# Kernel optimization log

Hardware: AMD Instinct MI355X
Metric: run time of the kernel (lower is better)

The kernel has to match this reference:

```python
import jax, jax.numpy as jnp
import numpy as np

D_MODEL = 1024
D_FF = 4096
NUM_EXPERTS = 8
TOP_K = 2


def setup_inputs() -> dict:
    key = jax.random.key(0)
    ks = jax.random.split(key, 9)
    s_in = 1.0 / np.sqrt(D_MODEL)
    s_ff = 1.0 / np.sqrt(D_FF)
    return {
        "x": jax.random.normal(ks[0], (2, 1024, D_MODEL), dtype=jnp.float32),
        "Wg": jax.random.uniform(ks[1], (D_MODEL, NUM_EXPERTS), minval=-s_in, maxval=s_in, dtype=jnp.float32),
        "bg": jax.random.uniform(ks[2], (NUM_EXPERTS,), minval=-s_in, maxval=s_in, dtype=jnp.float32),
        "W1": jax.random.uniform(ks[3], (NUM_EXPERTS, D_MODEL, D_FF), minval=-s_in, maxval=s_in, dtype=jnp.float32),
        "b1": jax.random.uniform(ks[4], (NUM_EXPERTS, D_FF), minval=-s_in, maxval=s_in, dtype=jnp.float32),
        "W2": jax.random.uniform(ks[5], (NUM_EXPERTS, D_MODEL, D_FF), minval=-s_in, maxval=s_in, dtype=jnp.float32),
        "b2": jax.random.uniform(ks[6], (NUM_EXPERTS, D_FF), minval=-s_in, maxval=s_in, dtype=jnp.float32),
        "W3": jax.random.uniform(ks[7], (NUM_EXPERTS, D_FF, D_MODEL), minval=-s_ff, maxval=s_ff, dtype=jnp.float32),
        "b3": jax.random.uniform(ks[8], (NUM_EXPERTS, D_MODEL), minval=-s_ff, maxval=s_ff, dtype=jnp.float32),
    }


def reference(x, Wg, bg, W1, b1, W2, b2, W3, b3):
    B, S, D = x.shape
    xf = x.reshape(-1, D)                                   # [N, D]
    N = xf.shape[0]

    # ---- Router (eval mode: no noise) ----
    logits = xf @ Wg + bg                                   # [N, E]
    top_logits, top_idx = jax.lax.top_k(logits, TOP_K)      # [N, K]
    top_w = jax.nn.softmax(top_logits, axis=-1)             # softmax over the top-k logits
    # scatter top-k weights into dense [N, E]; indices are unique per row
    comb_w = jnp.zeros_like(logits).at[jnp.arange(N)[:, None], top_idx].set(top_w)

    # ---- Experts: GLU-MLP, dense per-expert (weights are 0 for unrouted tokens) ----
    h1 = jnp.einsum('nd,edf->enf', xf, W1) + b1[:, None, :]  # [E, N, F]
    h2 = jnp.einsum('nd,edf->enf', xf, W2) + b2[:, None, :]
    hidden = jax.nn.gelu(h1, approximate=False) * h2         # torch nn.GELU is exact (erf)
    expert_out = jnp.einsum('enf,efd->end', hidden, W3) + b3[:, None, :]  # [E, N, D]

    # ---- Weighted combine ----
    final = jnp.einsum('end,ne->nd', expert_out, comb_w)     # [N, D]
    aux_loss = 0.0  # eval mode: aux loss inactive
    return final.reshape(B, S, D), aux_loss
```

## Files before the change

### kernel.cpp

```cpp
#include <hip/hip_runtime.h>
#include <hip/hip_bf16.h>
#include <math.h>

#define D_MODEL 1024
#define D_FF    4096
#define NE      8
#define MT      256

typedef __bf16 bf16x8 __attribute__((ext_vector_type(8)));
typedef float  f32x4  __attribute__((ext_vector_type(4)));

__device__ __forceinline__ void async16(const void* g, void* l) {
    __builtin_amdgcn_global_load_lds(
        (__attribute__((address_space(1))) uint32_t*)g,
        (__attribute__((address_space(3))) uint32_t*)l, 16, 0, 0);
}

__device__ __forceinline__ void transpose_tile_k128(
    const float* __restrict__ s, __bf16* __restrict__ d,
    int K, int N, int kt, int nt, int tid, float (*tile)[65])
{
    int tr = tid >> 4, tc = (tid & 15) * 4;
#pragma unroll
    for (int p = 0; p < 8; ++p) {
        float4 v = *reinterpret_cast<const float4*>(
            s + (size_t)(kt + tr + p * 16) * N + nt + tc);
        tile[tr + p * 16][tc + 0] = v.x;
        tile[tr + p * 16][tc + 1] = v.y;
        tile[tr + p * 16][tc + 2] = v.z;
        tile[tr + p * 16][tc + 3] = v.w;
    }
    __syncthreads();
    int kq = (tid & 15) * 8;
#pragma unroll
    for (int p = 0; p < 4; ++p) {
        int rr = (tid >> 4) + p * 16;
        bf16x8 pk;
#pragma unroll
        for (int i = 0; i < 8; ++i) pk[i] = (__bf16)tile[kq + i][rr];
        *reinterpret_cast<bf16x8*>(d + (size_t)(nt + rr) * K + kt + kq) = pk;
    }
}

__global__ __launch_bounds__(256) void fused_pre(
    const float* __restrict__ x, const float* __restrict__ Wg,
    const float* __restrict__ bg, int* __restrict__ topidx,
    float* __restrict__ topw, __bf16* __restrict__ Xb,
    const float* __restrict__ W1, const float* __restrict__ W2,
    const float* __restrict__ W3,
    __bf16* __restrict__ W1t, __bf16* __restrict__ W2t,
    __bf16* __restrict__ W3t, int nrouter)
{
    __shared__ float buf[128][65];
    int bid = blockIdx.x, tid = threadIdx.x;

    if (bid >= nrouter) {
        int tt = bid - nrouter;
        if (tt < 2 * 4096) {
            const float* s = W1; __bf16* d = W1t;
            if (tt >= 4096) { s = W2; d = W2t; tt -= 4096; }
            int e = tt >> 9, rem = tt & 511;
            int kt_i = rem >> 6, nt_i = rem & 63;
            transpose_tile_k128(s + ((size_t)e << 22), d + ((size_t)e << 22),
                                D_MODEL, D_FF, kt_i * 128, nt_i * 64, tid, buf);
        } else {
            tt -= 2 * 4096;
            int e = tt >> 9, rem = tt & 511;
            int kt_i = rem >> 4, nt_i = rem & 15;
            transpose_tile_k128(W3 + ((size_t)e << 22), W3t + ((size_t)e << 22),
                                D_FF, D_MODEL, kt_i * 128, nt_i * 64, tid, buf);
        }
        return;
    }

    int n = bid;
    const float* xr = x + (size_t)n * D_MODEL;
    int d0 = tid * 4;
    float4 xv = *reinterpret_cast<const float4*>(xr + d0);

    union { __bf16 h[4]; ushort4 u; } pk;
    pk.h[0] = (__bf16)xv.x; pk.h[1] = (__bf16)xv.y;
    pk.h[2] = (__bf16)xv.z; pk.h[3] = (__bf16)xv.w;
    *reinterpret_cast<ushort4*>(Xb + (size_t)n * D_MODEL + d0) = pk.u;

    float part[NE];
#pragma unroll
    for (int e = 0; e < NE; ++e) part[e] = 0.f;
    float xs[4] = {xv.x, xv.y, xv.z, xv.w};
#pragma unroll
    for (int j = 0; j < 4; ++j) {
        const float4* wr = reinterpret_cast<const float4*>(Wg + (size_t)(d0 + j) * NE);
        float4 w0 = wr[0], w1 = wr[1];
        part[0] += xs[j] * w0.x; part[1] += xs[j] * w0.y;
        part[2] += xs[j] * w0.z; part[3] += xs[j] * w0.w;
        part[4] += xs[j] * w1.x; part[5] += xs[j] * w1.y;
        part[6] += xs[j] * w1.z; part[7] += xs[j] * w1.w;
    }
#pragma unroll
    for (int off = 32; off > 0; off >>= 1) {
#pragma unroll
        for (int e = 0; e < NE; ++e) part[e] += __shfl_down(part[e], off);
    }
    float* sred = &buf[0][0];
    float* slog = &buf[1][0];
    int wave = tid >> 6, lane = tid & 63;
    if (lane == 0) {
#pragma unroll
        for (int e = 0; e < NE; ++e) sred[wave * NE + e] = part[e];
    }
    __syncthreads();
    if (tid < NE)
        slog[tid] = bg[tid] + sred[tid] + sred[NE + tid] + sred[2 * NE + tid] + sred[3 * NE + tid];
    __syncthreads();
    if (tid == 0) {
        float m0 = -1e30f, m1 = -1e30f; int i0 = 0, i1 = 0;
        for (int e = 0; e < NE; ++e) {
            float l = slog[e];
            if (l > m0)      { m1 = m0; i1 = i0; m0 = l; i0 = e; }
            else if (l > m1) { m1 = l;  i1 = e; }
        }
        float w1 = expf(m1 - m0);
        float s  = 1.f + w1;
        topidx[n * 2 + 0] = i0; topidx[n * 2 + 1] = i1;
        topw[n * 2 + 0] = 1.f / s; topw[n * 2 + 1] = w1 / s;
    }
}

__global__ __launch_bounds__(256) void build_lists_kernel(
    const int* __restrict__ topidx, const float* __restrict__ topw,
    int* __restrict__ pairTok, float* __restrict__ pairW,
    int* __restrict__ rbe, int* __restrict__ pairRow,
    int npairs, int maxrows, int maxblk)
{
    __shared__ int cnt[NE], cur[NE], pof[NE];
    int tid = threadIdx.x;
    if (tid < NE) { cnt[tid] = 0; cur[tid] = 0; }
    for (int i = tid; i < maxrows; i += 256) pairTok[i] = -1;
    for (int i = tid; i < maxblk; i += 256) rbe[i] = -1;
    __syncthreads();
    for (int p = tid; p < npairs; p += 256) atomicAdd(&cnt[topidx[p]], 1);
    __syncthreads();
    if (tid == 0) {
        int off = 0;
        for (int e = 0; e < NE; ++e) { pof[e] = off; off += (cnt[e] + MT - 1) & ~(MT - 1); }
        for (int e = 0; e < NE; ++e) {
            int nb = (cnt[e] + MT - 1) / MT;
            for (int j = 0; j < nb; ++j) rbe[pof[e] / MT + j] = e;
        }
    }
    __syncthreads();
    for (int p = tid; p < npairs; p += 256) {
        int e = topidx[p];
        int pos = atomicAdd(&cur[e], 1);
        int r = pof[e] + pos;
        pairTok[r]  = p >> 1;
        pairW[r]    = topw[p];
        pairRow[p]  = r;
    }
}

__global__ __launch_bounds__(512) void gemm1_mfma(
    const __bf16* __restrict__ Xb, const __bf16* __restrict__ W1t,
    const __bf16* __restrict__ W2t, const float* __restrict__ b1,
    const float* __restrict__ b2, const int* __restrict__ pairTok,
    const int* __restrict__ rbe, const __bf16* __restrict__ zpg,
    __bf16* __restrict__ hidden)
{
    int b = blockIdx.x;
    int e = rbe[b];
    if (e < 0) return;
    int fblk = blockIdx.y * 128;

    __shared__ __bf16 smem[2][32768];

    int tid = threadIdx.x, w = tid >> 6, l = tid & 63;
    int srcslot = (l & 7) ^ (l >> 3);
    int r0 = b * MT;

    const __bf16* aptr[4];
#pragma unroll
    for (int j = 0; j < 4; ++j) {
        int row = w * 32 + j * 8 + (l >> 3);
        int tok = pairTok[r0 + row];
        aptr[j] = (tok >= 0 ? Xb + (size_t)tok * D_MODEL : zpg) + srcslot * 8;
    }
    const __bf16* b1base = W1t + ((size_t)e << 22)
        + (size_t)(fblk + w * 16 + (l >> 3)) * D_MODEL + srcslot * 8;
    const __bf16* b2base = W2t + ((size_t)e << 22)
        + (size_t)(fblk + w * 16 + (l >> 3)) * D_MODEL + srcslot * 8;

    int wm = (w >> 1) * 64, wf = (w & 1) * 64;
    int lm = l & 15;

    f32x4 c1[4][4], c2[4][4];
#pragma unroll
    for (int mi = 0; mi < 4; ++mi)
#pragma unroll
        for (int fj = 0; fj < 4; ++fj) {
            c1[mi][fj] = (f32x4){0.f, 0.f, 0.f, 0.f};
            c2[mi][fj] = (f32x4){0.f, 0.f, 0.f, 0.f};
        }

    auto stage = [&](int buf, int k0) {
        __bf16* base = &smem[buf][0];
#pragma unroll
        for (int j = 0; j < 4; ++j)
            async16(aptr[j] + k0, base + w * 2048 + j * 512);
        async16(b1base + k0,               base + 16384 + w * 1024);
        async16(b1base + 8 * D_MODEL + k0, base + 16384 + w * 1024 + 512);
        async16(b2base + k0,               base + 24576 + w * 1024);
        async16(b2base + 8 * D_MODEL + k0, base + 24576 + w * 1024 + 512);
    };

    stage(0, 0);
    __syncthreads();
    const int NT = D_MODEL / 64;
    for (int t = 0; t < NT; ++t) {
        int cur = t & 1;
        if (t + 1 < NT) stage(cur ^ 1, (t + 1) * 64);
        const __bf16* sb = &smem[cur][0];
#pragma unroll
        for (int ks = 0; ks < 2; ++ks) {
            int sl = (((ks * 4 + (l >> 4)) ^ (l & 7)) << 3);
            bf16x8 a[4];
#pragma unroll
            for (int mi = 0; mi < 4; ++mi)
                a[mi] = *reinterpret_cast<const bf16x8*>(sb + (wm + mi * 16 + lm) * 64 + sl);
#pragma unroll
            for (int fj = 0; fj < 4; ++fj) {
                int frow = wf + fj * 16 + lm;
                bf16x8 bv1 = *reinterpret_cast<const bf16x8*>(sb + 16384 + frow * 64 + sl);
                bf16x8 bv2 = *reinterpret_cast<const bf16x8*>(sb + 24576 + frow * 64 + sl);
#pragma unroll
                for (int mi = 0; mi < 4; ++mi) {
                    c1[mi][fj] = __builtin_amdgcn_mfma_f32_16x16x32_bf16(a[mi], bv1, c1[mi][fj], 0, 0, 0);
                    c2[mi][fj] = __builtin_amdgcn_mfma_f32_16x16x32_bf16(a[mi], bv2, c2[mi][fj], 0, 0, 0);
                }
            }
        }
        __syncthreads();
    }

#pragma unroll
    for (int fj = 0; fj < 4; ++fj) {
        int f = fblk + wf + fj * 16 + lm;
        float b1v = b1[e * D_FF + f];
        float b2v = b2[e * D_FF + f];
#pragma unroll
        for (int mi = 0; mi < 4; ++mi)
#pragma unroll
            for (int r = 0; r < 4; ++r) {
                int m = wm + mi * 16 + (l >> 4) * 4 + r;
                float h1 = c1[mi][fj][r] + b1v;
                float h2 = c2[mi][fj][r] + b2v;
                float g = 0.5f * h1 * (1.f + erff(h1 * 0.70710678118654752f));
                hidden[(size_t)(r0 + m) * D_FF + f] = (__bf16)(g * h2);
            }
    }
}

__global__ __launch_bounds__(512, 4) void gemm2_mfma(
    const __bf16* __restrict__ hidden, const __bf16* __restrict__ W3t,
    const float* __restrict__ b3, const int* __restrict__ rbe,
    float* __restrict__ po)
{
    int rb = blockIdx.x;
    int e = rbe[rb >> 1];
    if (e < 0) return;
    int dblk = blockIdx.y * 128;

    __shared__ __bf16 smem[2][16384];

    int tid = threadIdx.x, w = tid >> 6, l = tid & 63;
    int ss8 = (l & 7) ^ (l >> 3);
    int r0m = rb * 128;

    const __bf16* abase = hidden + (size_t)(r0m + w * 16 + (l >> 3)) * D_FF + ss8 * 8;
    const __bf16* bbase = W3t + ((size_t)e << 22)
        + (size_t)(dblk + w * 16 + (l >> 3)) * D_FF + ss8 * 8;

    int wm = (w >> 1) * 32, wn = (w & 1) * 64;
    int lm = l & 15;

    f32x4 c[2][4];
#pragma unroll
    for (int mi = 0; mi < 2; ++mi)
#pragma unroll
        for (int nj = 0; nj < 4; ++nj) c[mi][nj] = (f32x4){0.f, 0.f, 0.f, 0.f};

    auto stage = [&](int buf, int k0) {
        __bf16* base = &smem[buf][0];
        async16(abase + k0,              base + w * 1024 + l * 8);
        async16(abase + 8 * D_FF + k0,   base + w * 1024 + 512 + l * 8);
        async16(bbase + k0,              base + 8192 + w * 1024 + l * 8);
        async16(bbase + 8 * D_FF + k0,   base + 8192 + w * 1024 + 512 + l * 8);
    };

    stage(0, 0);
    __syncthreads();
    const int NT = D_FF / 64;
    for (int t = 0; t < NT; ++t) {
        int cur = t & 1;
        if (t + 1 < NT) stage(cur ^ 1, (t + 1) * 64);
        const __bf16* sb = &smem[cur][0];
#pragma unroll
        for (int ks = 0; ks < 2; ++ks) {
            int sl = (((ks * 4 + (l >> 4)) ^ (l & 7)) << 3);
            bf16x8 a[2];
#pragma unroll
            for (int mi = 0; mi < 2; ++mi)
                a[mi] = *reinterpret_cast<const bf16x8*>(sb + (wm + mi * 16 + lm) * 64 + sl);
#pragma unroll
            for (int nj = 0; nj < 4; ++nj) {
                bf16x8 bv = *reinterpret_cast<const bf16x8*>(sb + 8192 + (wn + nj * 16 + lm) * 64 + sl);
#pragma unroll
                for (int mi = 0; mi < 2; ++mi)
                    c[mi][nj] = __builtin_amdgcn_mfma_f32_16x16x32_bf16(a[mi], bv, c[mi][nj], 0, 0, 0);
            }
        }
        __syncthreads();
    }

#pragma unroll
    for (int nj = 0; nj < 4; ++nj) {
        int d = dblk + wn + nj * 16 + lm;
        float b3v = b3[e * D_MODEL + d];
#pragma unroll
        for (int mi = 0; mi < 2; ++mi)
#pragma unroll
            for (int r = 0; r < 4; ++r) {
                int m = wm + mi * 16 + (l >> 4) * 4 + r;
                po[(size_t)(r0m + m) * D_MODEL + d] = c[mi][nj][r] + b3v;
            }
    }
}

__global__ __launch_bounds__(256) void combine_kernel(
    const float* __restrict__ po, const float* __restrict__ topw,
    const int* __restrict__ pairRow, float* __restrict__ out)
{
    int t = blockIdx.x, tid = threadIdx.x;
    int d = tid * 4;
    float w0 = topw[t * 2], w1 = topw[t * 2 + 1];
    int r0 = pairRow[t * 2], r1 = pairRow[t * 2 + 1];
    float4 v0 = *reinterpret_cast<const float4*>(po + (size_t)r0 * D_MODEL + d);
    float4 v1 = *reinterpret_cast<const float4*>(po + (size_t)r1 * D_MODEL + d);
    float4 o;
    o.x = w0 * v0.x + w1 * v1.x;
    o.y = w0 * v0.y + w1 * v1.y;
    o.z = w0 * v0.z + w1 * v1.z;
    o.w = w0 * v0.w + w1 * v1.w;
    *reinterpret_cast<float4*>(out + (size_t)t * D_MODEL + d) = o;
}

extern "C" void kernel_launch(void* const* d_in, const int* in_sizes, int n_in,
                              void* d_out, int out_size, void* d_ws, size_t ws_size,
                              hipStream_t stream)
{
    const float* x  = (const float*)d_in[0];
    const float* Wg = (const float*)d_in[1];
    const float* bg = (const float*)d_in[2];
    const float* W1 = (const float*)d_in[3];
    const float* b1 = (const float*)d_in[4];
    const float* W2 = (const float*)d_in[5];
    const float* b2 = (const float*)d_in[6];
    const float* W3 = (const float*)d_in[7];
    const float* b3 = (const float*)d_in[8];
    float* out = (float*)d_out;

    int N = in_sizes[0] / D_MODEL;
    int npairs = N * 2;
    int maxblk = npairs / MT + NE;
    int maxrows = maxblk * MT;

    char* ws = (char*)d_ws;
    size_t off = 0;
    auto alloc = [&](size_t bytes) -> void* {
        void* p = ws + off;
        off = (off + bytes + 255) & ~(size_t)255;
        return p;
    };
    int*    topidx  = (int*)   alloc((size_t)npairs * 4);
    float*  topw    = (float*) alloc((size_t)npairs * 4);
    int*    pairTok = (int*)   alloc((size_t)maxrows * 4);
    float*  pairW   = (float*) alloc((size_t)maxrows * 4);
    int*    rbe     = (int*)   alloc((size_t)maxblk * 4);
    int*    pairRow = (int*)   alloc((size_t)npairs * 4);
    __bf16* Xb      = (__bf16*)alloc((size_t)N * D_MODEL * 2);
    __bf16* hidden  = (__bf16*)alloc((size_t)maxrows * D_FF * 2);
    __bf16* zpg     = (__bf16*)alloc(4096);
    const size_t WSZ = (size_t)NE * D_MODEL * D_FF * 2;
    __bf16* W1t = (__bf16*)alloc(WSZ);
    __bf16* W2t = (__bf16*)alloc(WSZ);
    __bf16* W3t = (__bf16*)alloc(WSZ);
    float*  po  = (float*)W1t;
    (void)ws_size; (void)n_in; (void)pairW;

    hipMemsetAsync(zpg, 0, 4096, stream);

    fused_pre<<<N + 3 * 4096, 256, 0, stream>>>(
        x, Wg, bg, topidx, topw, Xb, W1, W2, W3, W1t, W2t, W3t, N);
    build_lists_kernel<<<1, 256, 0, stream>>>(topidx, topw, pairTok, pairW, rbe,
                                              pairRow, npairs, maxrows, maxblk);
    gemm1_mfma<<<dim3(maxblk, D_FF / 128), 512, 0, stream>>>(
        Xb, W1t, W2t, b1, b2, pairTok, rbe, zpg, hidden);
    gemm2_mfma<<<dim3(maxblk * 2, D_MODEL / 128), 512, 0, stream>>>(
        hidden, W3t, b3, rbe, po);
    combine_kernel<<<N, 256, 0, stream>>>(po, topw, pairRow, out);
}
```

Measured before the change: 335.6 us.

## Restructure gate/up GEMM main loop with deeper prefetch and phased MFMA scheduling

The main loop of the fused W1/W2 GEMM now prefetches two K-tiles ahead instead of one. It uses explicit s_waitcnt vmcnt counts and raw s_barrier in place of __syncthreads, so global→LDS async loads overlap a full iteration of compute. The B1 and B2 MFMA blocks are split into separate phases, each preceded by its own B-fragment loads, raised with s_setprio, and separated by workgroup barriers so that waves interleave. This aims to hide memory latency and cut register pressure, at the cost of more barriers per iteration and dependence on hand-counted vmcnt values.

New measurement: 342.3 us. 2.0% more time.

```diff
diff --git a/kernel.cpp b/kernel.cpp
--- a/kernel.cpp
+++ b/kernel.cpp
@@ -213,32 +213,51 @@
     };
 
     stage(0, 0);
-    __syncthreads();
+    stage(1, 64);
+    asm volatile("s_waitcnt vmcnt(8)" ::: "memory");
+    __builtin_amdgcn_s_barrier();
+
     const int NT = D_MODEL / 64;
     for (int t = 0; t < NT; ++t) {
         int cur = t & 1;
-        if (t + 1 < NT) stage(cur ^ 1, (t + 1) * 64);
         const __bf16* sb = &smem[cur][0];
 #pragma unroll
         for (int ks = 0; ks < 2; ++ks) {
             int sl = (((ks * 4 + (l >> 4)) ^ (l & 7)) << 3);
-            bf16x8 a[4];
+            bf16x8 a[4], bv[4];
 #pragma unroll
             for (int mi = 0; mi < 4; ++mi)
                 a[mi] = *reinterpret_cast<const bf16x8*>(sb + (wm + mi * 16 + lm) * 64 + sl);
 #pragma unroll
-            for (int fj = 0; fj < 4; ++fj) {
-                int frow = wf + fj * 16 + lm;
-                bf16x8 bv1 = *reinterpret_cast<const bf16x8*>(sb + 16384 + frow * 64 + sl);
-                bf16x8 bv2 = *reinterpret_cast<const bf16x8*>(sb + 24576 + frow * 64 + sl);
-#pragma unroll
-                for (int mi = 0; mi < 4; ++mi) {
-                    c1[mi][fj] = __builtin_amdgcn_mfma_f32_16x16x32_bf16(a[mi], bv1, c1[mi][fj], 0, 0, 0);
-                    c2[mi][fj] = __builtin_amdgcn_mfma_f32_16x16x32_bf16(a[mi], bv2, c2[mi][fj], 0, 0, 0);
-                }
-            }
-        }
-        __syncthreads();
+            for (int fj = 0; fj < 4; ++fj)
+                bv[fj] = *reinterpret_cast<const bf16x8*>(sb + 16384 + (wf + fj * 16 + lm) * 64 + sl);
+            __builtin_amdgcn_s_setprio(1);
+#pragma unroll
+            for (int fj = 0; fj < 4; ++fj)
+#pragma unroll
+                for (int mi = 0; mi < 4; ++mi)
+                    c1[mi][fj] = __builtin_amdgcn_mfma_f32_16x16x32_bf16(a[mi], bv[fj], c1[mi][fj], 0, 0, 0);
+            __builtin_amdgcn_s_setprio(0);
+            __builtin_amdgcn_s_barrier();
+#pragma unroll
+            for (int fj = 0; fj < 4; ++fj)
+                bv[fj] = *reinterpret_cast<const bf16x8*>(sb + 24576 + (wf + fj * 16 + lm) * 64 + sl);
+            __builtin_amdgcn_s_setprio(1);
+#pragma unroll
+            for (int fj = 0; fj < 4; ++fj)
+#pragma unroll
+                for (int mi = 0; mi < 4; ++mi)
+                    c2[mi][fj] = __builtin_amdgcn_mfma_f32_16x16x32_bf16(a[mi], bv[fj], c2[mi][fj], 0, 0, 0);
+            __builtin_amdgcn_s_setprio(0);
+            __builtin_amdgcn_s_barrier();
+        }
+        if (t + 2 < NT) {
+            stage(cur, (t + 2) * 64);
+            asm volatile("s_waitcnt vmcnt(8)" ::: "memory");
+        } else if (t + 1 < NT) {
+            asm volatile("s_waitcnt vmcnt(0)" ::: "memory");
+        }
+        __builtin_amdgcn_s_barrier();
     }
 
 #pragma unroll
```
